# Performance work log

Measured on AMD Instinct MI355X. Metric: run time of the kernel, lower is better.

The kernel has to match this reference:

```python
import jax, jax.numpy as jnp
import numpy as np

N = 50000
E = 800000
IN_DIM, HID, OUT = 64, 256, 128


def gcn_conv(x, edge_index, W, b):
    """PyG GCNConv with add_self_loops=False, sym normalization, unit edge weights.
    Transform-then-propagate: out[i] = sum_{e: col[e]=i} norm[e] * (x @ W)[row[e]] + b
    norm[e] = deg^-1/2[row] * deg^-1/2[col], deg = in-degree at col.
    """
    n = x.shape[0]
    row, col = edge_index[0], edge_index[1]
    xw = x @ W  # [N, out]
    deg = jax.ops.segment_sum(jnp.ones(row.shape[0], dtype=x.dtype), col, num_segments=n)
    dis = jnp.where(deg > 0, jax.lax.rsqrt(jnp.where(deg > 0, deg, 1.0)), 0.0)
    norm = dis[row] * dis[col]  # [E]
    msg = xw[row] * norm[:, None]  # [E, out]
    out = jax.ops.segment_sum(msg, col, num_segments=n)
    return out + b


def setup_inputs() -> dict:
    key = jax.random.key(0)
    ks = jax.random.split(key, 16)
    def lin(k, fi, fo):
        s = 1.0 / np.sqrt(fi)
        k1, k2 = jax.random.split(k)
        return (jax.random.uniform(k1, (fi, fo), jnp.float32, -s, s),
                jax.random.uniform(k2, (fo,), jnp.float32, -s, s))
    x = jax.random.normal(ks[0], (N, IN_DIM), jnp.float32)
    edge_index = jax.random.randint(ks[1], (2, E), 0, N, dtype=jnp.int64)
    w_fc, b_fc = lin(ks[2], IN_DIM, HID)
    w_conv1, b_conv1 = lin(ks[3], IN_DIM, HID)
    w_fc1, b_fc1 = lin(ks[4], 2 * HID, OUT)
    w_conv2, b_conv2 = lin(ks[5], 2 * HID, OUT)
    w_fc2, b_fc2 = lin(ks[6], OUT, 1)
    w_conv3, b_conv3 = lin(ks[7], OUT, 1)
    return dict(x=x, edge_index=edge_index,
                w_fc=w_fc, b_fc=b_fc, w_conv1=w_conv1, b_conv1=b_conv1,
                w_fc1=w_fc1, b_fc1=b_fc1, w_conv2=w_conv2, b_conv2=b_conv2,
                w_fc2=w_fc2, b_fc2=b_fc2, w_conv3=w_conv3, b_conv3=b_conv3)


def reference(x, edge_index, w_fc, b_fc, w_conv1, b_conv1, w_fc1, b_fc1,
              w_conv2, b_conv2, w_fc2, b_fc2, w_conv3, b_conv3):
    # MTGCL gcn_mlp, eval mode (dropout / dropout_adj are identity)
    x1 = jax.nn.relu(x @ w_fc + b_fc)                       # [N, HID]
    x2 = jax.nn.relu(gcn_conv(x, edge_index, w_conv1, b_conv1))  # [N, HID]
    x3 = jnp.concatenate((x1, x2), axis=1)                  # [N, 2*HID]
    x5 = jax.nn.relu(x3 @ w_fc1 + b_fc1)                    # [N, OUT]
    x6 = jax.nn.relu(gcn_conv(x3, edge_index, w_conv2, b_conv2))
    x7 = x5 + x6                                            # [N, OUT]
    pre = (x7 @ w_fc2 + b_fc2) + gcn_conv(x7, edge_index, w_conv3, b_conv3)
    return pre  # [N, 1]
```

## Files before the change

### kernel.cpp

```cpp
#include <hip/hip_runtime.h>
#include <hip/hip_bf16.h>

typedef __attribute__((ext_vector_type(8))) short short8;
typedef __attribute__((ext_vector_type(4))) float f32x4;

__device__ __forceinline__ ushort bf16_bits(float v) {
    __hip_bfloat16 h = __float2bfloat16(v);
    return *reinterpret_cast<ushort*>(&h);
}
__device__ __forceinline__ float bf16_val(float v) {
    __hip_bfloat16 h = __float2bfloat16(v);
    return __bfloat162float(h);
}
__device__ __forceinline__ float bfu_lo(uint u) {
    uint t = u << 16; return __uint_as_float(t);
}
__device__ __forceinline__ float bfu_hi(uint u) {
    uint t = u & 0xffff0000u; return __uint_as_float(t);
}


__global__ __launch_bounds__(256) void k_setup(const int* __restrict__ col,
                                               int* __restrict__ bcnt, int E, int nbc,
                                               const float* __restrict__ w0,
                                               const float* __restrict__ w1,
                                               const float* __restrict__ wf1,
                                               const float* __restrict__ wf2,
                                               ushort* __restrict__ W0f,
                                               ushort* __restrict__ W1f,
                                               ushort* __restrict__ Bf) {
    if ((int)blockIdx.x < nbc) {
        __shared__ int hist[196];
        int tid = threadIdx.x;
        int base = blockIdx.x * 2048;
        if (tid < 196) hist[tid] = 0;
        __syncthreads();
        #pragma unroll
        for (int i = 0; i < 8; i++) {
            int e = base + i * 256 + tid;
            if (e < E) atomicAdd(&hist[col[e] >> 8], 1);
        }
        __syncthreads();
        if (tid < 196 && hist[tid] > 0) atomicAdd(&bcnt[tid], hist[tid]);
        return;
    }
    int id = (blockIdx.x - nbc) * 256 + threadIdx.x;
    if (id < 8192) {
        int mat = id >> 12;
        int rem = id & 4095;
        int lane = rem & 63;
        int nt = (rem >> 6) & 15;
        int k0i = (rem >> 10) & 1;
        int arr = rem >> 11;
        const float* w = mat ? w1 : w0;
        ushort* dst = mat ? W1f : W0f;
        int n = nt * 16 + (lane & 15);
        int kb = k0i * 32 + (lane >> 4) * 8;
        ushort o[8];
        #pragma unroll
        for (int j = 0; j < 8; j++) {
            float v = w[(size_t)(kb + j) * 256 + n];
            o[j] = arr ? bf16_bits(v - bf16_val(v)) : bf16_bits(v);
        }
        *reinterpret_cast<int4*>(&dst[(size_t)rem * 8]) = *reinterpret_cast<const int4*>(o);
    } else if (id < 24576) {
        int rem = id - 8192;
        int lane = rem & 63;
        int nt   = (rem >> 6) & 15;
        int k0i  = (rem >> 10) & 15;
        int n = nt * 16 + (lane & 15);
        int kbase = k0i * 32 + (lane >> 4) * 8;
        ushort outv[8];
        #pragma unroll
        for (int j = 0; j < 8; j++) {
            int k = kbase + j;
            float v = (n < 128) ? wf1[(size_t)k * 128 + n]
                                : wf2[(size_t)k * 128 + (n - 128)];
            outv[j] = bf16_bits(v);
        }
        *reinterpret_cast<int4*>(&Bf[(size_t)rem * 8]) = *reinterpret_cast<const int4*>(outv);
    }
}

__global__ __launch_bounds__(256) void k_bscan(const int* __restrict__ bcnt,
                                               int* __restrict__ bbase,
                                               int* __restrict__ bcur, int E) {
    int i = threadIdx.x;
    int v = (i < 196) ? bcnt[i] : 0;
    int lane = i & 63, w = i >> 6;
    int s = v;
    #pragma unroll
    for (int o = 1; o < 64; o <<= 1) {
        int t = __shfl_up(s, o);
        if (lane >= o) s += t;
    }
    __shared__ int wsum[4];
    if (lane == 63) wsum[w] = s;
    __syncthreads();
    int add = 0;
    for (int ww = 0; ww < w; ww++) add += wsum[ww];
    int excl = s + add - v;
    if (i < 196) {
        bbase[i] = excl;
        bcur[i] = excl;
    }
    if (i == 195) bbase[196] = excl + v;
}

__global__ __launch_bounds__(256) void k_binA(const int* __restrict__ row,
                                              const int* __restrict__ col,
                                              int* __restrict__ bcur,
                                              uint* __restrict__ stage, int E) {
    __shared__ uint colbuf[2048];
    __shared__ int hist[196];
    __shared__ int lcur[196];
    int tid = threadIdx.x;
    int base = blockIdx.x * 2048;
    if (tid < 196) hist[tid] = 0;
    __syncthreads();
    #pragma unroll
    for (int i = 0; i < 8; i++) {
        int e = base + i * 256 + tid;
        uint c = 0xFFFFFFFFu;
        if (e < E) {
            c = (uint)col[e];
            atomicAdd(&hist[c >> 8], 1);
        }
        colbuf[i * 256 + tid] = c;
    }
    __syncthreads();
    if (tid < 196 && hist[tid] > 0) lcur[tid] = atomicAdd(&bcur[tid], hist[tid]);
    __syncthreads();
    #pragma unroll
    for (int i = 0; i < 8; i++) {
        int idx = i * 256 + tid;
        uint c = colbuf[idx];
        if (c != 0xFFFFFFFFu) {
            uint r = (uint)row[base + idx];
            int p = atomicAdd(&lcur[c >> 8], 1);
            stage[p] = (c << 16) | r;
        }
    }
}

__global__ __launch_bounds__(256) void k_binB(const uint* __restrict__ stage,
                                              const int* __restrict__ bbase,
                                              int* __restrict__ rowptr,
                                              float* __restrict__ dis,
                                              ushort* __restrict__ csr16,
                                              int n, int E) {
    __shared__ int cnt[256];
    __shared__ int cur[256];
    __shared__ int wsum[4];
    int b = blockIdx.x;
    int lo = b << 8;
    int tid = threadIdx.x;
    int gstart = bbase[b], gend = bbase[b + 1];
    cnt[tid] = 0;
    __syncthreads();
    for (int idx = gstart + tid; idx < gend; idx += 256)
        atomicAdd(&cnt[(stage[idx] >> 16) & 255], 1);
    __syncthreads();
    int v = cnt[tid];
    int lane = tid & 63, w = tid >> 6;
    int s = v;
    #pragma unroll
    for (int o = 1; o < 64; o <<= 1) {
        int t = __shfl_up(s, o);
        if (lane >= o) s += t;
    }
    if (lane == 63) wsum[w] = s;
    __syncthreads();
    int add = 0;
    for (int ww = 0; ww < w; ww++) add += wsum[ww];
    int excl = s + add - v + gstart;
    int node = lo + tid;
    if (node < n) {
        rowptr[node] = excl;
        dis[node] = v > 0 ? rsqrtf((float)v) : 0.f;
    }
    cur[tid] = excl;
    if (tid == 0 && b == gridDim.x - 1) rowptr[n] = E;
    __syncthreads();
    for (int idx = gstart + tid; idx < gend; idx += 256) {
        uint pk = stage[idx];
        int p = atomicAdd(&cur[(pk >> 16) & 255], 1);
        csr16[p] = (ushort)(pk & 0xffffu);
    }
}


__global__ __launch_bounds__(256) void k_prepX(const float* __restrict__ x,
                                               const float* __restrict__ dis,
                                               ushort* __restrict__ xh,
                                               ushort* __restrict__ xs, int total4) {
    int i = blockIdx.x * 256 + threadIdx.x;
    if (i >= total4) return;
    float4 v = reinterpret_cast<const float4*>(x)[i];
    float dn = dis[i >> 4];
    float vv[4] = {v.x, v.y, v.z, v.w};
    uint hv[2], sv[2];
    #pragma unroll
    for (int g = 0; g < 2; g++) {
        float a0 = vv[g * 2], a1 = vv[g * 2 + 1];
        hv[g] = (uint)bf16_bits(a0) | ((uint)bf16_bits(a1) << 16);
        sv[g] = (uint)bf16_bits(a0 * dn) | ((uint)bf16_bits(a1 * dn) << 16);
    }
    reinterpret_cast<uint2*>(xh)[i] = make_uint2(hv[0], hv[1]);
    reinterpret_cast<uint2*>(xs)[i] = make_uint2(sv[0], sv[1]);
}


__global__ __launch_bounds__(256) void k_agg64_csr(const ushort* __restrict__ xs,
                                                   const int* __restrict__ rowptr,
                                                   const ushort* __restrict__ csr16,
                                                   const float* __restrict__ dis,
                                                   ushort* __restrict__ agghi, int n) {
    int node = blockIdx.x * 4 + (threadIdx.x >> 6);
    if (node >= n) return;
    int lane = threadIdx.x & 63;
    int sub = lane >> 3;
    int li  = lane & 7;
    int s = rowptr[node], t = rowptr[node + 1];
    float acc[8] = {};
    int p = s;
    for (; p + 16 <= t; p += 16) {
        int rr[2];
        #pragma unroll
        for (int u = 0; u < 2; u++) rr[u] = csr16[p + u * 8 + sub];
        uint4 v[2];
        #pragma unroll
        for (int u = 0; u < 2; u++)
            v[u] = *reinterpret_cast<const uint4*>(&xs[(size_t)rr[u] * 64 + li * 8]);
        #pragma unroll
        for (int u = 0; u < 2; u++) {
            acc[0] += bfu_lo(v[u].x); acc[1] += bfu_hi(v[u].x);
            acc[2] += bfu_lo(v[u].y); acc[3] += bfu_hi(v[u].y);
            acc[4] += bfu_lo(v[u].z); acc[5] += bfu_hi(v[u].z);
            acc[6] += bfu_lo(v[u].w); acc[7] += bfu_hi(v[u].w);
        }
    }
    for (; p < t; p += 8) {
        int e = p + sub;
        if (e < t) {
            int rr = csr16[e];
            uint4 v = *reinterpret_cast<const uint4*>(&xs[(size_t)rr * 64 + li * 8]);
            acc[0] += bfu_lo(v.x); acc[1] += bfu_hi(v.x);
            acc[2] += bfu_lo(v.y); acc[3] += bfu_hi(v.y);
            acc[4] += bfu_lo(v.z); acc[5] += bfu_hi(v.z);
            acc[6] += bfu_lo(v.w); acc[7] += bfu_hi(v.w);
        }
    }
    #pragma unroll
    for (int j = 0; j < 8; j++) {
        acc[j] += __shfl_xor(acc[j], 8);
        acc[j] += __shfl_xor(acc[j], 16);
        acc[j] += __shfl_xor(acc[j], 32);
    }
    if (sub == 0) {
        float dn = dis[node];
        uint hp[4];
        #pragma unroll
        for (int g = 0; g < 4; g++) {
            float a0 = acc[g * 2] * dn, a1 = acc[g * 2 + 1] * dn;
            hp[g] = (uint)bf16_bits(a0) | ((uint)bf16_bits(a1) << 16);
        }
        *reinterpret_cast<uint4*>(&agghi[(size_t)node * 64 + li * 8]) =
            make_uint4(hp[0], hp[1], hp[2], hp[3]);
    }
}

__global__ __launch_bounds__(256) void k_agg128_x7dot(
    const ushort* __restrict__ xw,
    const int* __restrict__ rowptr,
    const ushort* __restrict__ csr16,
    const float* __restrict__ dis,
    const float* __restrict__ b2,
    const ushort* __restrict__ x5,
    const float* __restrict__ wfc2, const float* __restrict__ bfc2,
    const float* __restrict__ wc3,  const float* __restrict__ bc3,
    float* __restrict__ out, float* __restrict__ xw3, int n) {
    int node = blockIdx.x * 4 + (threadIdx.x >> 6);
    if (node >= n) return;
    int lane = threadIdx.x & 63;
    int sub = lane >> 4;
    int li  = lane & 15;
    int s = rowptr[node], t = rowptr[node + 1];
    float acc[8] = {};
    int p = s;
    for (; p + 16 <= t; p += 16) {
        int rr[4];
        #pragma unroll
        for (int u = 0; u < 4; u++) rr[u] = csr16[p + u * 4 + sub];
        uint4 v[4];
        #pragma unroll
        for (int u = 0; u < 4; u++)
            v[u] = *reinterpret_cast<const uint4*>(&xw[(size_t)rr[u] * 128 + li * 8]);
        #pragma unroll
        for (int u = 0; u < 4; u++) {
            acc[0] += bfu_lo(v[u].x); acc[1] += bfu_hi(v[u].x);
            acc[2] += bfu_lo(v[u].y); acc[3] += bfu_hi(v[u].y);
            acc[4] += bfu_lo(v[u].z); acc[5] += bfu_hi(v[u].z);
            acc[6] += bfu_lo(v[u].w); acc[7] += bfu_hi(v[u].w);
        }
    }
    for (; p < t; p += 4) {
        int e = p + sub;
        if (e < t) {
            int rr = csr16[e];
            uint4 v = *reinterpret_cast<const uint4*>(&xw[(size_t)rr * 128 + li * 8]);
            acc[0] += bfu_lo(v.x); acc[1] += bfu_hi(v.x);
            acc[2] += bfu_lo(v.y); acc[3] += bfu_hi(v.y);
            acc[4] += bfu_lo(v.z); acc[5] += bfu_hi(v.z);
            acc[6] += bfu_lo(v.w); acc[7] += bfu_hi(v.w);
        }
    }
    #pragma unroll
    for (int j = 0; j < 8; j++) {
        acc[j] += __shfl_xor(acc[j], 16);
        acc[j] += __shfl_xor(acc[j], 32);
    }
    float dn = dis[node];
    float s1 = 0.f, s2 = 0.f;
    if (sub == 0) {
        uint4 xv = *reinterpret_cast<const uint4*>(&x5[(size_t)node * 128 + li * 8]);
        float xr[8] = {bfu_lo(xv.x), bfu_hi(xv.x), bfu_lo(xv.y), bfu_hi(xv.y),
                       bfu_lo(xv.z), bfu_hi(xv.z), bfu_lo(xv.w), bfu_hi(xv.w)};
        #pragma unroll
        for (int j = 0; j < 8; j++) {
            int d = li * 8 + j;
            float x7 = xr[j] + fmaxf(dn * acc[j] + b2[d], 0.f);
            s1 += x7 * wfc2[d];
            s2 += x7 * wc3[d];
        }
    }
    #pragma unroll
    for (int o = 32; o > 0; o >>= 1) {
        s1 += __shfl_down(s1, o);
        s2 += __shfl_down(s2, o);
    }
    if (lane == 0) {
        out[node] = s1 + bfc2[0] + bc3[0];
        xw3[node] = s2 * dn;
    }
}

__global__ __launch_bounds__(256) void k_agg1_csr(const float* __restrict__ sv,
                                                  const int* __restrict__ rowptr,
                                                  const ushort* __restrict__ csr16,
                                                  const float* __restrict__ dis,
                                                  float* __restrict__ out, int n) {
    int i = blockIdx.x * 256 + threadIdx.x;
    if (i >= n) return;
    int s = rowptr[i], t = rowptr[i + 1];
    float a = 0.f;
    #pragma unroll 4
    for (int p = s; p < t; ++p) a += sv[csr16[p]];
    out[i] += dis[i] * a;
}

__device__ __forceinline__ int x3_swz(int inner) {
    return inner ^ ((((inner >> 6) & 1) << 4) ^ (((inner >> 7) & 1) << 3));
}

__global__ __launch_bounds__(512) void k_mmfused(
    const ushort* __restrict__ xh, const ushort* __restrict__ ah_,
    const ushort* __restrict__ W0f, const ushort* __restrict__ W1f,
    const float* __restrict__ b0, const float* __restrict__ b1,
    const ushort* __restrict__ Bf, const float* __restrict__ bias1,
    const float* __restrict__ dis,
    ushort* __restrict__ C1, ushort* __restrict__ C2, int M) {
    __shared__ ushort x3[4 * 16 * 512];

    const int t = threadIdx.x;
    const int lane = t & 63;
    const int wv = t >> 6;
    const int m0 = blockIdx.x * 64;
    const int ln15 = lane & 15;
    const int quad = lane >> 4;

    f32x4 acc[4][2];

    #pragma unroll
    for (int layer = 0; layer < 2; layer++) {
        const ushort* A = layer ? ah_ : xh;
        const ushort* Wf = layer ? W1f : W0f;
        const float* bias = layer ? b1 : b0;
        #pragma unroll
        for (int mt = 0; mt < 4; mt++)
            #pragma unroll
            for (int ntl = 0; ntl < 2; ntl++)
                acc[mt][ntl] = (f32x4){0.f, 0.f, 0.f, 0.f};

        short8 wh[2][2], wl[2][2], av[2][4];
        #pragma unroll
        for (int k0i = 0; k0i < 2; k0i++) {
            #pragma unroll
            for (int ntl = 0; ntl < 2; ntl++) {
                const ushort* pw = Wf + ((size_t)k0i * 16 + wv * 2 + ntl) * 512 + (size_t)lane * 8;
                wh[k0i][ntl] = *reinterpret_cast<const short8*>(pw);
                wl[k0i][ntl] = *reinterpret_cast<const short8*>(pw + 16384);
            }
            #pragma unroll
            for (int mt = 0; mt < 4; mt++) {
                int gm = m0 + mt * 16 + ln15;
                int gmc = gm < M - 1 ? gm : M - 1;
                size_t ia = (size_t)gmc * 64 + k0i * 32 + quad * 8;
                av[k0i][mt] = *reinterpret_cast<const short8*>(&A[ia]);
            }
        }
        #pragma unroll
        for (int k0i = 0; k0i < 2; k0i++) {
            #pragma unroll
            for (int mt = 0; mt < 4; mt++) {
                #pragma unroll
                for (int ntl = 0; ntl < 2; ntl++)
                    acc[mt][ntl] = __builtin_amdgcn_mfma_f32_16x16x32_bf16(av[k0i][mt], wh[k0i][ntl], acc[mt][ntl], 0, 0, 0);
                #pragma unroll
                for (int ntl = 0; ntl < 2; ntl++)
                    acc[mt][ntl] = __builtin_amdgcn_mfma_f32_16x16x32_bf16(av[k0i][mt], wl[k0i][ntl], acc[mt][ntl], 0, 0, 0);
            }
        }

        #pragma unroll
        for (int mt = 0; mt < 4; mt++) {
            #pragma unroll
            for (int ntl = 0; ntl < 2; ntl++) {
                int gn = (wv * 2 + ntl) * 16 + ln15;
                int gcol = gn + layer * 256;
                int k0f = gcol >> 5, qf = (gcol >> 3) & 3, j = gcol & 7;
                #pragma unroll
                for (int r = 0; r < 4; r++) {
                    int rloc = quad * 4 + r;
                    float v = fmaxf(acc[mt][ntl][r] + bias[gn], 0.f);
                    int inner = x3_swz((qf * 16 + rloc) * 8 + j);
                    x3[(mt * 16 + k0f) * 512 + inner] = bf16_bits(v);
                }
            }
        }
    }
    __syncthreads();

    #pragma unroll
    for (int mt = 0; mt < 4; mt++)
        #pragma unroll
        for (int ntl = 0; ntl < 2; ntl++)
            acc[mt][ntl] = (f32x4){0.f, 0.f, 0.f, 0.f};

    const int innerA = x3_swz(lane * 8);
    const ushort* bPtr = Bf + ((size_t)wv * 2) * 512 + (size_t)lane * 8;

    auto ldB = [&](int k0, short8* dst) {
        #pragma unroll
        for (int ntl = 0; ntl < 2; ntl++)
            dst[ntl] = *reinterpret_cast<const short8*>(bPtr + ((size_t)k0 * 16 + ntl) * 512);
    };
    auto ldA = [&](int k0, short8* dst) {
        #pragma unroll
        for (int mt = 0; mt < 4; mt++)
            dst[mt] = *reinterpret_cast<const short8*>(&x3[(mt * 16 + k0) * 512 + innerA]);
    };

    short8 b0r[2], b1r[2], b2r[2], b3r[2];
    short8 aC[4], aN[4];
    ldB(0, b0r); ldB(1, b1r); ldB(2, b2r); ldB(3, b3r);
    ldA(0, aC);

    #pragma unroll
    for (int k4 = 0; k4 < 4; k4++) {
        #pragma unroll
        for (int j = 0; j < 4; j++) {
            const int k0 = k4 * 4 + j;
            short8* bcur = (j == 0) ? b0r : (j == 1) ? b1r : (j == 2) ? b2r : b3r;
            short8 tB[2];
            int kpre = k0 + 4 < 16 ? k0 + 4 : 0;
            ldB(kpre, tB);
            int ka = k0 + 1 < 16 ? k0 + 1 : 0;
            ldA(ka, aN);
            #pragma unroll
            for (int mt = 0; mt < 4; mt++)
                #pragma unroll
                for (int ntl = 0; ntl < 2; ntl++)
                    acc[mt][ntl] = __builtin_amdgcn_mfma_f32_16x16x32_bf16(aC[mt], bcur[ntl], acc[mt][ntl], 0, 0, 0);
            bcur[0] = tB[0]; bcur[1] = tB[1];
            #pragma unroll
            for (int mt = 0; mt < 4; mt++) aC[mt] = aN[mt];
        }
    }
    __syncthreads();

    #pragma unroll
    for (int mt = 0; mt < 4; mt++) {
        float dn[4];
        #pragma unroll
        for (int r = 0; r < 4; r++) {
            int gm = m0 + mt * 16 + quad * 4 + r;
            dn[r] = (gm < M) ? dis[gm] : 0.f;
        }
        #pragma unroll
        for (int ntl = 0; ntl < 2; ntl++) {
            int gn = (wv * 2 + ntl) * 16 + ln15;
            #pragma unroll
            for (int r = 0; r < 4; r++) {
                int row64 = mt * 16 + quad * 4 + r;
                float v = acc[mt][ntl][r];
                ushort ov = (gn < 128) ? bf16_bits(fmaxf(v + bias1[gn], 0.f))
                                       : bf16_bits(v * dn[r]);
                int idx = row64 * 256 + gn;
                idx ^= ((row64 >> 2) & 3) << 4;
                x3[idx] = ov;
            }
        }
    }
    __syncthreads();

    #pragma unroll
    for (int c = 0; c < 4; c++) {
        int offu = c * 4096 + t * 8;
        int row64 = offu >> 8;
        int colu = offu & 255;
        int src = row64 * 256 + (colu ^ (((row64 >> 2) & 3) << 4));
        uint4 v = *reinterpret_cast<const uint4*>(&x3[src]);
        int gm = m0 + row64;
        if (gm < M) {
            if (colu < 128)
                *reinterpret_cast<uint4*>(&C1[(size_t)gm * 128 + colu]) = v;
            else
                *reinterpret_cast<uint4*>(&C2[(size_t)gm * 128 + (colu - 128)]) = v;
        }
    }
}

extern "C" void kernel_launch(void* const* d_in, const int* in_sizes, int n_in,
                              void* d_out, int out_size, void* d_ws, size_t ws_size,
                              hipStream_t stream) {
    const float* x       = (const float*)d_in[0];
    const int*   ei      = (const int*)d_in[1];
    const float* w_fc    = (const float*)d_in[2];
    const float* b_fc    = (const float*)d_in[3];
    const float* w_conv1 = (const float*)d_in[4];
    const float* b_conv1 = (const float*)d_in[5];
    const float* w_fc1   = (const float*)d_in[6];
    const float* b_fc1   = (const float*)d_in[7];
    const float* w_conv2 = (const float*)d_in[8];
    const float* b_conv2 = (const float*)d_in[9];
    const float* w_fc2   = (const float*)d_in[10];
    const float* b_fc2   = (const float*)d_in[11];
    const float* w_conv3 = (const float*)d_in[12];
    const float* b_conv3 = (const float*)d_in[13];

    const int N = in_sizes[0] / 64;
    const int E = in_sizes[1] / 2;
    const int* row = ei;
    const int* col = ei + E;

    const int nb = (N + 255) / 256;
    const int nbc = (E + 2047) / 2048;
    const int nblk = (N + 63) / 64;

    char* p = (char*)d_ws;
    auto alloc = [&](size_t elems) {
        void* q = p; p += ((elems + 3) & ~(size_t)3) * 4; return q;
    };
    int*    bcnt    = (int*)   alloc(200);
    int*    bbase   = (int*)   alloc(200);
    int*    bcur    = (int*)   alloc(200);
    int*    rowptr  = (int*)   alloc(N + 4);
    uint*   stage   = (uint*)  alloc(E);
    ushort* csr16   = (ushort*)alloc((size_t)E / 2);
    float*  dis     = (float*) alloc(N);
    ushort* xh      = (ushort*)alloc((size_t)N * 32);
    ushort* xs      = (ushort*)alloc((size_t)N * 32);
    ushort* agghi   = (ushort*)alloc((size_t)N * 32);
    ushort* Bf      = (ushort*)alloc(65536);
    ushort* W0f     = (ushort*)alloc(16384);
    ushort* W1f     = (ushort*)alloc(16384);
    ushort* x5      = (ushort*)alloc((size_t)N * 64);
    ushort* xw2     = (ushort*)alloc((size_t)N * 64);
    float*  xw3     = (float*) alloc(N);

    float* out = (float*)d_out;

    hipMemsetAsync(bcnt, 0, 196 * sizeof(int), stream);
    k_setup<<<nbc + 96, 256, 0, stream>>>(col, bcnt, E, nbc,
                                          w_fc, w_conv1, w_fc1, w_conv2,
                                          W0f, W1f, Bf);
    k_bscan<<<1, 256, 0, stream>>>(bcnt, bbase, bcur, E);
    k_binA<<<(E + 2047) / 2048, 256, 0, stream>>>(row, col, bcur, stage, E);
    k_binB<<<nb, 256, 0, stream>>>(stage, bbase, rowptr, dis, csr16, N, E);

    k_prepX<<<(N * 16 + 255) / 256, 256, 0, stream>>>(x, dis, xh, xs, N * 16);

    k_agg64_csr<<<(N + 3) / 4, 256, 0, stream>>>(xs, rowptr, csr16, dis, agghi, N);

    k_mmfused<<<nblk, 512, 0, stream>>>(xh, agghi, W0f, W1f, b_fc, b_conv1,
                                        Bf, b_fc1, dis, x5, xw2, N);

    k_agg128_x7dot<<<(N + 3) / 4, 256, 0, stream>>>(
        xw2, rowptr, csr16, dis, b_conv2, x5,
        w_fc2, b_fc2, w_conv3, b_conv3, out, xw3, N);

    k_agg1_csr<<<(N + 255) / 256, 256, 0, stream>>>(xw3, rowptr, csr16, dis, out, N);
}
```

Measured before the change: 243.2 us.

## Fold bucket scan into binning kernels, fuse X prep into binB, parallelize agg1

```diff
diff --git a/kernel.cpp b/kernel.cpp
--- a/kernel.cpp
+++ b/kernel.cpp
@@ -82,38 +82,15 @@
     }
 }
 
-__global__ __launch_bounds__(256) void k_bscan(const int* __restrict__ bcnt,
-                                               int* __restrict__ bbase,
-                                               int* __restrict__ bcur, int E) {
-    int i = threadIdx.x;
-    int v = (i < 196) ? bcnt[i] : 0;
-    int lane = i & 63, w = i >> 6;
-    int s = v;
-    #pragma unroll
-    for (int o = 1; o < 64; o <<= 1) {
-        int t = __shfl_up(s, o);
-        if (lane >= o) s += t;
-    }
-    __shared__ int wsum[4];
-    if (lane == 63) wsum[w] = s;
-    __syncthreads();
-    int add = 0;
-    for (int ww = 0; ww < w; ww++) add += wsum[ww];
-    int excl = s + add - v;
-    if (i < 196) {
-        bbase[i] = excl;
-        bcur[i] = excl;
-    }
-    if (i == 195) bbase[196] = excl + v;
-}
-
 __global__ __launch_bounds__(256) void k_binA(const int* __restrict__ row,
                                               const int* __restrict__ col,
+                                              const int* __restrict__ bcnt,
                                               int* __restrict__ bcur,
                                               uint* __restrict__ stage, int E) {
     __shared__ uint colbuf[2048];
     __shared__ int hist[196];
     __shared__ int lcur[196];
+    __shared__ int wsum[4];
     int tid = threadIdx.x;
     int base = blockIdx.x * 2048;
     if (tid < 196) hist[tid] = 0;
@@ -129,7 +106,21 @@
         colbuf[i * 256 + tid] = c;
     }
     __syncthreads();
-    if (tid < 196 && hist[tid] > 0) lcur[tid] = atomicAdd(&bcur[tid], hist[tid]);
+    int v = (tid < 196) ? bcnt[tid] : 0;
+    int lane = tid & 63, w = tid >> 6;
+    int s = v;
+    #pragma unroll
+    for (int o = 1; o < 64; o <<= 1) {
+        int t2 = __shfl_up(s, o);
+        if (lane >= o) s += t2;
+    }
+    if (lane == 63) wsum[w] = s;
+    __syncthreads();
+    int add = 0;
+    for (int ww = 0; ww < w; ww++) add += wsum[ww];
+    int excl = s + add - v;
+    if (tid < 196 && hist[tid] > 0)
+        lcur[tid] = excl + atomicAdd(&bcur[tid], hist[tid]);
     __syncthreads();
     #pragma unroll
     for (int i = 0; i < 8; i++) {
@@ -144,20 +135,42 @@
 }
 
 __global__ __launch_bounds__(256) void k_binB(const uint* __restrict__ stage,
-                                              const int* __restrict__ bbase,
+                                              const int* __restrict__ bcnt,
                                               int* __restrict__ rowptr,
                                               float* __restrict__ dis,
                                               ushort* __restrict__ csr16,
+                                              const float* __restrict__ x,
+                                              ushort* __restrict__ xh,
+                                              ushort* __restrict__ xs,
                                               int n, int E) {
     __shared__ int cnt[256];
     __shared__ int cur[256];
     __shared__ int wsum[4];
+    __shared__ int sgse[2];
+    __shared__ float sdis[256];
     int b = blockIdx.x;
     int lo = b << 8;
     int tid = threadIdx.x;
-    int gstart = bbase[b], gend = bbase[b + 1];
+
+    {
+        int v = (tid < 196) ? bcnt[tid] : 0;
+        int lane = tid & 63, w = tid >> 6;
+        int s = v;
+        #pragma unroll
+        for (int o = 1; o < 64; o <<= 1) {
+            int t2 = __shfl_up(s, o);
+            if (lane >= o) s += t2;
+        }
+        if (lane == 63) wsum[w] = s;
+        __syncthreads();
+        int add = 0;
+        for (int ww = 0; ww < w; ww++) add += wsum[ww];
+        int excl = s + add - v;
+        if (tid == b) { sgse[0] = excl; sgse[1] = excl + v; }
+    }
     cnt[tid] = 0;
     __syncthreads();
+    int gstart = sgse[0], gend = sgse[1];
     for (int idx = gstart + tid; idx < gend; idx += 256)
         atomicAdd(&cnt[(stage[idx] >> 16) & 255], 1);
     __syncthreads();
@@ -166,8 +179,8 @@
     int s = v;
     #pragma unroll
     for (int o = 1; o < 64; o <<= 1) {
-        int t = __shfl_up(s, o);
-        if (lane >= o) s += t;
+        int t2 = __shfl_up(s, o);
+        if (lane >= o) s += t2;
     }
     if (lane == 63) wsum[w] = s;
     __syncthreads();
@@ -175,10 +188,12 @@
     for (int ww = 0; ww < w; ww++) add += wsum[ww];
     int excl = s + add - v + gstart;
     int node = lo + tid;
+    float d = v > 0 ? rsqrtf((float)v) : 0.f;
     if (node < n) {
         rowptr[node] = excl;
-        dis[node] = v > 0 ? rsqrtf((float)v) : 0.f;
-    }
+        dis[node] = d;
+    }
+    sdis[tid] = d;
     cur[tid] = excl;
     if (tid == 0 && b == gridDim.x - 1) rowptr[n] = E;
     __syncthreads();
@@ -187,27 +202,26 @@
         int p = atomicAdd(&cur[(pk >> 16) & 255], 1);
         csr16[p] = (ushort)(pk & 0xffffu);
     }
-}
-
-
-__global__ __launch_bounds__(256) void k_prepX(const float* __restrict__ x,
-                                               const float* __restrict__ dis,
-                                               ushort* __restrict__ xh,
-                                               ushort* __restrict__ xs, int total4) {
-    int i = blockIdx.x * 256 + threadIdx.x;
-    if (i >= total4) return;
-    float4 v = reinterpret_cast<const float4*>(x)[i];
-    float dn = dis[i >> 4];
-    float vv[4] = {v.x, v.y, v.z, v.w};
-    uint hv[2], sv[2];
-    #pragma unroll
-    for (int g = 0; g < 2; g++) {
-        float a0 = vv[g * 2], a1 = vv[g * 2 + 1];
-        hv[g] = (uint)bf16_bits(a0) | ((uint)bf16_bits(a1) << 16);
-        sv[g] = (uint)bf16_bits(a0 * dn) | ((uint)bf16_bits(a1 * dn) << 16);
-    }
-    reinterpret_cast<uint2*>(xh)[i] = make_uint2(hv[0], hv[1]);
-    reinterpret_cast<uint2*>(xs)[i] = make_uint2(sv[0], sv[1]);
+
+    #pragma unroll
+    for (int i = 0; i < 16; i++) {
+        int li = i * 256 + tid;
+        int nl = li >> 4;
+        if (lo + nl >= n) break;
+        size_t gf = (size_t)b * 4096 + li;
+        float4 vv = reinterpret_cast<const float4*>(x)[gf];
+        float dn = sdis[nl];
+        float a[4] = {vv.x, vv.y, vv.z, vv.w};
+        uint hv[2], sv[2];
+        #pragma unroll
+        for (int g = 0; g < 2; g++) {
+            float a0 = a[g * 2], a1 = a[g * 2 + 1];
+            hv[g] = (uint)bf16_bits(a0) | ((uint)bf16_bits(a1) << 16);
+            sv[g] = (uint)bf16_bits(a0 * dn) | ((uint)bf16_bits(a1 * dn) << 16);
+        }
+        reinterpret_cast<uint2*>(xh)[gf] = make_uint2(hv[0], hv[1]);
+        reinterpret_cast<uint2*>(xs)[gf] = make_uint2(sv[0], sv[1]);
+    }
 }
 
 
@@ -240,15 +254,26 @@
             acc[6] += bfu_lo(v[u].w); acc[7] += bfu_hi(v[u].w);
         }
     }
-    for (; p < t; p += 8) {
-        int e = p + sub;
-        if (e < t) {
-            int rr = csr16[e];
-            uint4 v = *reinterpret_cast<const uint4*>(&xs[(size_t)rr * 64 + li * 8]);
-            acc[0] += bfu_lo(v.x); acc[1] += bfu_hi(v.x);
-            acc[2] += bfu_lo(v.y); acc[3] += bfu_hi(v.y);
-            acc[4] += bfu_lo(v.z); acc[5] += bfu_hi(v.z);
-            acc[6] += bfu_lo(v.w); acc[7] += bfu_hi(v.w);
+    if (p < t) {
+        bool ok[2]; int rr[2];
+        #pragma unroll
+        for (int u = 0; u < 2; u++) {
+            int e = p + u * 8 + sub;
+            ok[u] = e < t;
+            rr[u] = csr16[ok[u] ? e : s];
+        }
+        uint4 v[2];
+        #pragma unroll
+        for (int u = 0; u < 2; u++)
+            v[u] = *reinterpret_cast<const uint4*>(&xs[(size_t)rr[u] * 64 + li * 8]);
+        #pragma unroll
+        for (int u = 0; u < 2; u++) {
+            if (ok[u]) {
+                acc[0] += bfu_lo(v[u].x); acc[1] += bfu_hi(v[u].x);
+                acc[2] += bfu_lo(v[u].y); acc[3] += bfu_hi(v[u].y);
+                acc[4] += bfu_lo(v[u].z); acc[5] += bfu_hi(v[u].z);
+                acc[6] += bfu_lo(v[u].w); acc[7] += bfu_hi(v[u].w);
+            }
         }
     }
     #pragma unroll
@@ -304,15 +329,26 @@
             acc[6] += bfu_lo(v[u].w); acc[7] += bfu_hi(v[u].w);
         }
     }
-    for (; p < t; p += 4) {
-        int e = p + sub;
-        if (e < t) {
-            int rr = csr16[e];
-            uint4 v = *reinterpret_cast<const uint4*>(&xw[(size_t)rr * 128 + li * 8]);
-            acc[0] += bfu_lo(v.x); acc[1] += bfu_hi(v.x);
-            acc[2] += bfu_lo(v.y); acc[3] += bfu_hi(v.y);
-            acc[4] += bfu_lo(v.z); acc[5] += bfu_hi(v.z);
-            acc[6] += bfu_lo(v.w); acc[7] += bfu_hi(v.w);
+    if (p < t) {
+        bool ok[4]; int rr[4];
+        #pragma unroll
+        for (int u = 0; u < 4; u++) {
+            int e = p + u * 4 + sub;
+            ok[u] = e < t;
+            rr[u] = csr16[ok[u] ? e : s];
+        }
+        uint4 v[4];
+        #pragma unroll
+        for (int u = 0; u < 4; u++)
+            v[u] = *reinterpret_cast<const uint4*>(&xw[(size_t)rr[u] * 128 + li * 8]);
+        #pragma unroll
+        for (int u = 0; u < 4; u++) {
+            if (ok[u]) {
+                acc[0] += bfu_lo(v[u].x); acc[1] += bfu_hi(v[u].x);
+                acc[2] += bfu_lo(v[u].y); acc[3] += bfu_hi(v[u].y);
+                acc[4] += bfu_lo(v[u].z); acc[5] += bfu_hi(v[u].z);
+                acc[6] += bfu_lo(v[u].w); acc[7] += bfu_hi(v[u].w);
+            }
         }
     }
     #pragma unroll
@@ -350,13 +386,17 @@
                                                   const ushort* __restrict__ csr16,
                                                   const float* __restrict__ dis,
                                                   float* __restrict__ out, int n) {
-    int i = blockIdx.x * 256 + threadIdx.x;
-    if (i >= n) return;
-    int s = rowptr[i], t = rowptr[i + 1];
+    int grp = threadIdx.x >> 4, l16 = threadIdx.x & 15;
+    int node = blockIdx.x * 16 + grp;
+    if (node >= n) return;
+    int s = rowptr[node], t = rowptr[node + 1];
     float a = 0.f;
-    #pragma unroll 4
-    for (int p = s; p < t; ++p) a += sv[csr16[p]];
-    out[i] += dis[i] * a;
+    for (int p = s + l16; p < t; p += 16) a += sv[csr16[p]];
+    a += __shfl_xor(a, 1);
+    a += __shfl_xor(a, 2);
+    a += __shfl_xor(a, 4);
+    a += __shfl_xor(a, 8);
+    if (l16 == 0) out[node] += dis[node] * a;
 }
 
 __device__ __forceinline__ int x3_swz(int inner) {
@@ -563,7 +603,6 @@
         void* q = p; p += ((elems + 3) & ~(size_t)3) * 4; return q;
     };
     int*    bcnt    = (int*)   alloc(200);
-    int*    bbase   = (int*)   alloc(200);
     int*    bcur    = (int*)   alloc(200);
     int*    rowptr  = (int*)   alloc(N + 4);
     uint*   stage   = (uint*)  alloc(E);
@@ -581,15 +620,13 @@
 
     float* out = (float*)d_out;
 
-    hipMemsetAsync(bcnt, 0, 196 * sizeof(int), stream);
+    hipMemsetAsync(bcnt, 0, 400 * sizeof(int), stream);
     k_setup<<<nbc + 96, 256, 0, stream>>>(col, bcnt, E, nbc,
                                           w_fc, w_conv1, w_fc1, w_conv2,
                                           W0f, W1f, Bf);
-    k_bscan<<<1, 256, 0, stream>>>(bcnt, bbase, bcur, E);
-    k_binA<<<(E + 2047) / 2048, 256, 0, stream>>>(row, col, bcur, stage, E);
-    k_binB<<<nb, 256, 0, stream>>>(stage, bbase, rowptr, dis, csr16, N, E);
-
-    k_prepX<<<(N * 16 + 255) / 256, 256, 0, stream>>>(x, dis, xh, xs, N * 16);
+    k_binA<<<nbc, 256, 0, stream>>>(row, col, bcnt, bcur, stage, E);
+    k_binB<<<nb, 256, 0, stream>>>(stage, bcnt, rowptr, dis, csr16,
+                                   x, xh, xs, N, E);
 
     k_agg64_csr<<<(N + 3) / 4, 256, 0, stream>>>(xs, rowptr, csr16, dis, agghi, N);
 
@@ -600,5 +637,5 @@
         xw2, rowptr, csr16, dis, b_conv2, x5,
         w_fc2, b_fc2, w_conv3, b_conv3, out, xw3, N);
 
-    k_agg1_csr<<<(N + 255) / 256, 256, 0, stream>>>(xw3, rowptr, csr16, dis, out, N);
-}
+    k_agg1_csr<<<(N + 15) / 16, 256, 0, stream>>>(xw3, rowptr, csr16, dis, out, N);
+}
```

Measured after the change: 241.1 us. No clear change (-0.9%).
